# Kernel tuning notes

Hardware: AMD Instinct MI355X
Metric: run time of the kernel (lower is better)

The kernel has to match this reference:

```python
import jax, jax.numpy as jnp
import numpy as np

N_NODES = 100000
N_EDGES = 1600000
N_FEAT = 128
HIDDEN = 64
N_LAYERS = 3


def setup_inputs() -> dict:
    key = jax.random.key(0)
    ks = jax.random.split(key, 8)
    x = jax.random.normal(ks[0], (N_NODES, N_FEAT), dtype=jnp.float32)
    edge_index = jax.random.randint(ks[1], (2, N_EDGES), 0, N_NODES, dtype=jnp.int64)
    s_emb = 1.0 / np.sqrt(N_FEAT)
    s_h = 1.0 / np.sqrt(HIDDEN)
    W_emb = jax.random.uniform(ks[2], (N_FEAT, HIDDEN), jnp.float32, -s_emb, s_emb)
    b_emb = jax.random.uniform(ks[3], (HIDDEN,), jnp.float32, -s_emb, s_emb)
    Ws = jax.random.uniform(ks[4], (N_LAYERS, HIDDEN, HIDDEN), jnp.float32, -s_h, s_h)
    bs = jax.random.uniform(ks[5], (N_LAYERS, HIDDEN), jnp.float32, -s_h, s_h)
    return {"x": x, "edge_index": edge_index, "W_emb": W_emb, "b_emb": b_emb,
            "Ws": Ws, "bs": bs}


def gcn_conv(h, src, dst, W, b, deg_inv_sqrt):
    # GCNConv with self-loops and symmetric normalization (PyG semantics):
    # out_i = sum_{j->i} d_i^{-1/2} d_j^{-1/2} (h_j W) + d_i^{-1} (h_i W) + b
    hw = h @ W                                   # [N, H]
    norm = deg_inv_sqrt[src] * deg_inv_sqrt[dst]  # [E]
    msg = hw[src] * norm[:, None]                 # [E, H] gather
    agg = jax.ops.segment_sum(msg, dst, num_segments=N_NODES)  # scatter-add
    agg = agg + hw * (deg_inv_sqrt * deg_inv_sqrt)[:, None]    # self-loop term
    return agg + b


def reference(x, edge_index, W_emb, b_emb, Ws, bs):
    src, dst = edge_index[0], edge_index[1]
    # degree with self-loops (edge weight 1), shared by every layer
    deg = jnp.zeros((N_NODES,), x.dtype).at[dst].add(1.0) + 1.0
    deg_inv_sqrt = jax.lax.rsqrt(deg)

    h = x @ W_emb + b_emb  # embedding Linear
    for i in range(N_LAYERS):
        h = jax.nn.relu(gcn_conv(h, src, dst, Ws[i], bs[i], deg_inv_sqrt))
    return h
```

## Files before the change

kernel.cpp:

```cpp
#include <hip/hip_runtime.h>
#include <hip/hip_fp16.h>
#include <math.h>

#define NN 100000
#define NE 1600000
#define NF 128
#define NH 64
#define NBUCK 196
#define CHA 8192
#define CAP 10240
#define NBLK 1563

typedef _Float16 f16x8 __attribute__((ext_vector_type(8)));
typedef float f32x4 __attribute__((ext_vector_type(4)));

__global__ __launch_bounds__(256) void part_bucket2(const int* __restrict__ src,
                                                    const int* __restrict__ dst,
                                                    int* __restrict__ bcnt,
                                                    int* __restrict__ tmp, int E) {
    __shared__ int hist[NBUCK];
    __shared__ int base[NBUCK];
    int t = threadIdx.x;
    int e0 = blockIdx.x * CHA;
    int e1 = min(e0 + CHA, E);
    if (t < NBUCK) hist[t] = 0;
    __syncthreads();
    for (int i = e0 + t; i < e1; i += 256) {
        atomicAdd(&hist[dst[i] >> 9], 1);
    }
    __syncthreads();
    if (t < NBUCK) {
        int h = hist[t];
        base[t] = h ? atomicAdd(&bcnt[t], h) : 0;
        hist[t] = 0;
    }
    __syncthreads();
    for (int i = e0 + t; i < e1; i += 256) {
        int d = dst[i];
        int b = d >> 9;
        int r = atomicAdd(&hist[b], 1);
        tmp[b * CAP + base[b] + r] = ((d & 511) << 17) | src[i];
    }
}

__global__ __launch_bounds__(256) void scan_buckets(const int* __restrict__ bcnt,
                                                    int* __restrict__ cbase,
                                                    int* __restrict__ rowptr) {
    __shared__ int s[256];
    int t = threadIdx.x;
    s[t] = (t < NBUCK) ? bcnt[t] : 0;
    __syncthreads();
    for (int off = 1; off < 256; off <<= 1) {
        int v = (t >= off) ? s[t - off] : 0;
        __syncthreads();
        s[t] += v;
        __syncthreads();
    }
    if (t < NBUCK) cbase[t] = (t == 0) ? 0 : s[t - 1];
    if (t == 0) rowptr[NN] = NE;
}

__global__ __launch_bounds__(256) void bucket_finalize(const int* __restrict__ bcnt,
                                                       const int* __restrict__ cbase,
                                                       const int* __restrict__ tmp,
                                                       int* __restrict__ rowptr,
                                                       float* __restrict__ dsq,
                                                       int* __restrict__ csr_src) {
    __shared__ int ebuf[CAP];
    __shared__ int hcnt[512];
    __shared__ int hoff[512];
    __shared__ int s[256];
    int b = blockIdx.x, t = threadIdx.x;
    int cb = bcnt[b];
    int base = cbase[b];
    const int* tsrc = tmp + b * CAP;
    for (int i = t; i < cb; i += 256) ebuf[i] = tsrc[i];
    hcnt[t] = 0;
    hcnt[t + 256] = 0;
    __syncthreads();
    for (int i = t; i < cb; i += 256) atomicAdd(&hcnt[ebuf[i] >> 17], 1);
    __syncthreads();
    int c0 = hcnt[2 * t], c1 = hcnt[2 * t + 1];
    s[t] = c0 + c1;
    __syncthreads();
    for (int off = 1; off < 256; off <<= 1) {
        int v = (t >= off) ? s[t - off] : 0;
        __syncthreads();
        s[t] += v;
        __syncthreads();
    }
    int pb = (t == 0) ? 0 : s[t - 1];
    hoff[2 * t] = pb;
    hoff[2 * t + 1] = pb + c0;
    __syncthreads();
    int nodelo = b << 9;
    int nnodes = min(512, NN - nodelo);
    for (int i = t; i < nnodes; i += 256) {
        rowptr[nodelo + i] = base + hoff[i];
        dsq[nodelo + i] = rsqrtf((float)hcnt[i] + 1.0f);
    }
    __syncthreads();
    for (int i = t; i < cb; i += 256) {
        int e = ebuf[i];
        int dlow = e >> 17;
        int p = atomicAdd(&hoff[dlow], 1);
        csr_src[base + p] = e & 0x1FFFF;
    }
}

__global__ __launch_bounds__(256) void combine_w(const float* __restrict__ We,
                                                 const float* __restrict__ be,
                                                 const float* __restrict__ W0,
                                                 _Float16* __restrict__ Wct,
                                                 float* __restrict__ bc) {
    __shared__ float w0[NH * NH];
    int t = threadIdx.x;
    for (int i = t; i < NH * NH; i += 256) w0[i] = W0[i];
    __syncthreads();
    int row = blockIdx.x * 4 + (t >> 6);
    int col = t & 63;
    float a = 0.f;
#pragma unroll 8
    for (int k = 0; k < NH; ++k) a += We[row * NH + k] * w0[k * NH + col];
    Wct[col * NF + row] = (_Float16)a;
    if (blockIdx.x == 0 && t < NH) {
        float s = 0.f;
        for (int k = 0; k < NH; ++k) s += be[k] * w0[k * NH + t];
        bc[t] = s;
    }
}

__global__ __launch_bounds__(256) void wconv(const float* __restrict__ W,
                                             _Float16* __restrict__ Wt) {
    int i = blockIdx.x * 256 + threadIdx.x;
    int k = i >> 6, c = i & 63;
    Wt[c * NH + k] = (_Float16)W[i];
}

__global__ __launch_bounds__(256) void fuse0_gemm(const float* __restrict__ x,
                                                  const _Float16* __restrict__ Wct,
                                                  const float* __restrict__ bc,
                                                  const float* __restrict__ dsq,
                                                  __half* __restrict__ hws) {
    __shared__ _Float16 sh[64 * NF];
    int t = threadIdx.x;
    int lane = t & 63;
    int w = t >> 6;
    int row0 = blockIdx.x * 64;

    f16x8 bf[4][4];
#pragma unroll
    for (int ct = 0; ct < 4; ++ct)
#pragma unroll
        for (int ks = 0; ks < 4; ++ks) {
            int col = ct * 16 + (lane & 15);
            int k = ks * 32 + (lane >> 4) * 8;
            bf[ct][ks] = *(const f16x8*)(Wct + col * NF + k);
        }

    const float4* xs = (const float4*)x;
#pragma unroll
    for (int i = 0; i < 8; ++i) {
        int f = t + i * 256;
        int r = f >> 5;
        int c4 = f & 31;
        int row = min(row0 + r, NN - 1);
        float4 v = xs[(size_t)row * 32 + c4];
        __half2 h0 = __floats2half2_rn(v.x, v.y);
        __half2 h1 = __floats2half2_rn(v.z, v.w);
        uint2 u;
        u.x = *(unsigned*)&h0;
        u.y = *(unsigned*)&h1;
        int byte = (r * 256 + c4 * 8) ^ ((r & 7) << 4);
        *(uint2*)((char*)sh + byte) = u;
    }
    __syncthreads();

    f32x4 acc[4] = {{0.f, 0.f, 0.f, 0.f}, {0.f, 0.f, 0.f, 0.f},
                    {0.f, 0.f, 0.f, 0.f}, {0.f, 0.f, 0.f, 0.f}};
    int ar = w * 16 + (lane & 15);
    int ak = (lane >> 4) * 8;
#pragma unroll
    for (int ks = 0; ks < 4; ++ks) {
        int byte = (ar * 256 + (ks * 32 + ak) * 2) ^ ((ar & 7) << 4);
        f16x8 af = *(const f16x8*)((const char*)sh + byte);
#pragma unroll
        for (int ct = 0; ct < 4; ++ct)
            acc[ct] = __builtin_amdgcn_mfma_f32_16x16x32_f16(af, bf[ct][ks], acc[ct], 0, 0, 0);
    }
#pragma unroll
    for (int ct = 0; ct < 4; ++ct) {
        int col = ct * 16 + (lane & 15);
        float bcv = bc[col];
#pragma unroll
        for (int r2 = 0; r2 < 4; ++r2) {
            int row = row0 + w * 16 + (lane >> 4) * 4 + r2;
            if (row < NN)
                hws[(size_t)row * NH + col] = __float2half((acc[ct][r2] + bcv) * dsq[row]);
        }
    }
}

__global__ __launch_bounds__(256) void layer_gemm(const __half* __restrict__ h,
                                                  const _Float16* __restrict__ Wt,
                                                  const float* __restrict__ dsq,
                                                  __half* __restrict__ hws) {
    __shared__ _Float16 sh[64 * NH];
    int t = threadIdx.x;
    int lane = t & 63;
    int w = t >> 6;
    int row0 = blockIdx.x * 64;

    f16x8 bf[4][2];
#pragma unroll
    for (int ct = 0; ct < 4; ++ct)
#pragma unroll
        for (int ks = 0; ks < 2; ++ks) {
            int col = ct * 16 + (lane & 15);
            int k = ks * 32 + (lane >> 4) * 8;
            bf[ct][ks] = *(const f16x8*)(Wt + col * NH + k);
        }

#pragma unroll
    for (int i = 0; i < 2; ++i) {
        int u = t + i * 256;
        int r = u >> 3;
        int c8 = u & 7;
        int row = min(row0 + r, NN - 1);
        uint4 v = *(const uint4*)(h + (size_t)row * NH + c8 * 8);
        int byte = (r * 128 + c8 * 16) ^ ((r & 7) << 4);
        *(uint4*)((char*)sh + byte) = v;
    }
    __syncthreads();

    f32x4 acc[4] = {{0.f, 0.f, 0.f, 0.f}, {0.f, 0.f, 0.f, 0.f},
                    {0.f, 0.f, 0.f, 0.f}, {0.f, 0.f, 0.f, 0.f}};
    int ar = w * 16 + (lane & 15);
    int ak = (lane >> 4) * 8;
#pragma unroll
    for (int ks = 0; ks < 2; ++ks) {
        int byte = (ar * 128 + (ks * 32 + ak) * 2) ^ ((ar & 7) << 4);
        f16x8 af = *(const f16x8*)((const char*)sh + byte);
#pragma unroll
        for (int ct = 0; ct < 4; ++ct)
            acc[ct] = __builtin_amdgcn_mfma_f32_16x16x32_f16(af, bf[ct][ks], acc[ct], 0, 0, 0);
    }
#pragma unroll
    for (int ct = 0; ct < 4; ++ct) {
        int col = ct * 16 + (lane & 15);
#pragma unroll
        for (int r2 = 0; r2 < 4; ++r2) {
            int row = row0 + w * 16 + (lane >> 4) * 4 + r2;
            if (row < NN)
                hws[(size_t)row * NH + col] = __float2half(acc[ct][r2] * dsq[row]);
        }
    }
}

#define ADDROWM(sidx, m)                                                     \
    {                                                                        \
        uint4 rv = *(const uint4*)(hws_in + (size_t)(sidx) * NH + fl);       \
        float2 f0 = __half22float2(*(const __half2*)&rv.x);                  \
        float2 f1 = __half22float2(*(const __half2*)&rv.y);                  \
        float2 f2 = __half22float2(*(const __half2*)&rv.z);                  \
        float2 f3 = __half22float2(*(const __half2*)&rv.w);                  \
        a0 += f0.x * (m); a1 += f0.y * (m); a2 += f1.x * (m); a3 += f1.y * (m); \
        a4 += f2.x * (m); a5 += f2.y * (m); a6 += f3.x * (m); a7 += f3.y * (m); \
    }

#define GATHER_BODY                                                          \
    int t = threadIdx.x;                                                     \
    int node = blockIdx.x * 4 + (t >> 6);                                    \
    int lane = t & 63;                                                       \
    int g = lane >> 3;                                                       \
    int fl = (lane & 7) << 3;                                                \
    int beg = rowptr[node], end = rowptr[node + 1];                          \
    int deg = end - beg;                                                     \
    float a0 = 0.f, a1 = 0.f, a2 = 0.f, a3 = 0.f;                            \
    float a4 = 0.f, a5 = 0.f, a6 = 0.f, a7 = 0.f;                            \
    if (g == 0) ADDROWM(node, 1.f);                                          \
    int idxl = csr_src[min(beg + lane, NE - 1)];                             \
    _Pragma("unroll")                                                        \
    for (int k = 0; k < 8; ++k) {                                            \
        if (k * 8 < deg) {                                                   \
            int e = k * 8 + g;                                               \
            int s_ = __shfl(idxl, min(e, deg - 1));                          \
            float m = (e < deg) ? 1.f : 0.f;                                 \
            ADDROWM(s_, m);                                                  \
        }                                                                    \
    }                                                                        \
    for (int jb = beg + 64; jb < end; jb += 64) {       \
        int rem = end - jb;                                                  \
        int idx2 = csr_src[min(jb + lane, NE - 1)];                          \
        _Pragma("unroll")                                                    \
        for (int k = 0; k < 8; ++k) {                                        \
            if (k * 8 < rem) {                                               \
                int e = k * 8 + g;                                           \
                int s_ = __shfl(idx2, min(e, rem - 1));                      \
                float m = (e < rem) ? 1.f : 0.f;                             \
                ADDROWM(s_, m);                                              \
            }                                                                \
        }                                                                    \
    }                                                                        \
    a0 += __shfl_xor(a0, 8);  a1 += __shfl_xor(a1, 8);                       \
    a2 += __shfl_xor(a2, 8);  a3 += __shfl_xor(a3, 8);                       \
    a4 += __shfl_xor(a4, 8);  a5 += __shfl_xor(a5, 8);                       \
    a6 += __shfl_xor(a6, 8);  a7 += __shfl_xor(a7, 8);                       \
    a0 += __shfl_xor(a0, 16); a1 += __shfl_xor(a1, 16);                      \
    a2 += __shfl_xor(a2, 16); a3 += __shfl_xor(a3, 16);                      \
    a4 += __shfl_xor(a4, 16); a5 += __shfl_xor(a5, 16);                      \
    a6 += __shfl_xor(a6, 16); a7 += __shfl_xor(a7, 16);                      \
    a0 += __shfl_xor(a0, 32); a1 += __shfl_xor(a1, 32);                      \
    a2 += __shfl_xor(a2, 32); a3 += __shfl_xor(a3, 32);                      \
    a4 += __shfl_xor(a4, 32); a5 += __shfl_xor(a5, 32);                      \
    a6 += __shfl_xor(a6, 32); a7 += __shfl_xor(a7, 32);

__global__ __launch_bounds__(256) void gather_h(const int* __restrict__ rowptr,
                                                const int* __restrict__ csr_src,
                                                const __half* __restrict__ hws_in,
                                                const float* __restrict__ dsq,
                                                const float* __restrict__ b,
                                                __half* __restrict__ hout) {
    GATHER_BODY
    if (lane < 8) {
        float ds = dsq[node];
        float4 b0 = *(const float4*)(b + fl);
        float4 b1 = *(const float4*)(b + fl + 4);
        __half2 o[4];
        o[0] = __floats2half2_rn(fmaxf(ds * a0 + b0.x, 0.f), fmaxf(ds * a1 + b0.y, 0.f));
        o[1] = __floats2half2_rn(fmaxf(ds * a2 + b0.z, 0.f), fmaxf(ds * a3 + b0.w, 0.f));
        o[2] = __floats2half2_rn(fmaxf(ds * a4 + b1.x, 0.f), fmaxf(ds * a5 + b1.y, 0.f));
        o[3] = __floats2half2_rn(fmaxf(ds * a6 + b1.z, 0.f), fmaxf(ds * a7 + b1.w, 0.f));
        *(uint4*)(hout + (size_t)node * NH + fl) = *(const uint4*)o;
    }
}

__global__ __launch_bounds__(256) void gather_out(const int* __restrict__ rowptr,
                                                  const int* __restrict__ csr_src,
                                                  const __half* __restrict__ hws_in,
                                                  const float* __restrict__ dsq,
                                                  const float* __restrict__ b,
                                                  float* __restrict__ outbuf) {
    GATHER_BODY
    if (lane < 8) {
        float ds = dsq[node];
        float4 b0 = *(const float4*)(b + fl);
        float4 b1 = *(const float4*)(b + fl + 4);
        float4 o0, o1;
        o0.x = fmaxf(ds * a0 + b0.x, 0.f);
        o0.y = fmaxf(ds * a1 + b0.y, 0.f);
        o0.z = fmaxf(ds * a2 + b0.z, 0.f);
        o0.w = fmaxf(ds * a3 + b0.w, 0.f);
        o1.x = fmaxf(ds * a4 + b1.x, 0.f);
        o1.y = fmaxf(ds * a5 + b1.y, 0.f);
        o1.z = fmaxf(ds * a6 + b1.z, 0.f);
        o1.w = fmaxf(ds * a7 + b1.w, 0.f);
        *(float4*)(outbuf + (size_t)node * NH + fl) = o0;
        *(float4*)(outbuf + (size_t)node * NH + fl + 4) = o1;
    }
}

extern "C" void kernel_launch(void* const* d_in, const int* in_sizes, int n_in,
                              void* d_out, int out_size, void* d_ws, size_t ws_size,
                              hipStream_t stream) {
    const float* x     = (const float*)d_in[0];
    const int*   ei    = (const int*)d_in[1];
    const float* W_emb = (const float*)d_in[2];
    const float* b_emb = (const float*)d_in[3];
    const float* Ws    = (const float*)d_in[4];
    const float* bs    = (const float*)d_in[5];
    float* out = (float*)d_out;

    const int* src = ei;
    const int* dst = ei + NE;

    char* w = (char*)d_ws;
    int*      bcnt    = (int*)w;              w += 256 * 4;
    int*      cbase   = (int*)w;              w += 256 * 4;
    int*      rowptr  = (int*)w;              w += (NN + 1) * 4;
    float*    dsq     = (float*)w;            w += NN * 4;
    float*    bc      = (float*)w;            w += NH * 4;
    _Float16* Wct     = (_Float16*)w;         w += NF * NH * 2;
    _Float16* Wt1     = (_Float16*)w;         w += NH * NH * 2;
    _Float16* Wt2     = (_Float16*)w;         w += NH * NH * 2;
    int*      csr_src = (int*)w;              w += NE * 4;
    int*      tmp     = (int*)w;              w += (size_t)NBUCK * CAP * 4;
    __half*   Bh      = (__half*)w;           w += (size_t)NN * NH * 2;
    __half*   H16     = (__half*)w;

    hipMemsetAsync(bcnt, 0, 256 * 4, stream);
    part_bucket2<<<(NE + CHA - 1) / CHA, 256, 0, stream>>>(src, dst, bcnt, tmp, NE);
    scan_buckets<<<1, 256, 0, stream>>>(bcnt, cbase, rowptr);
    bucket_finalize<<<NBUCK, 256, 0, stream>>>(bcnt, cbase, tmp, rowptr, dsq, csr_src);

    combine_w<<<NF / 4, 256, 0, stream>>>(W_emb, b_emb, Ws, Wct, bc);
    wconv<<<16, 256, 0, stream>>>(Ws + 1 * NH * NH, Wt1);
    wconv<<<16, 256, 0, stream>>>(Ws + 2 * NH * NH, Wt2);

    fuse0_gemm<<<NBLK, 256, 0, stream>>>(x, Wct, bc, dsq, Bh);

    gather_h<<<NN / 4, 256, 0, stream>>>(rowptr, csr_src, Bh, dsq, bs, H16);
    layer_gemm<<<NBLK, 256, 0, stream>>>(H16, Wt1, dsq, Bh);
    gather_h<<<NN / 4, 256, 0, stream>>>(rowptr, csr_src, Bh, dsq, bs + NH, H16);
    layer_gemm<<<NBLK, 256, 0, stream>>>(H16, Wt2, dsq, Bh);
    gather_out<<<NN / 4, 256, 0, stream>>>(rowptr, csr_src, Bh, dsq,
                                           bs + 2 * NH, out);
}
```

Baseline: 280.7 us.

## Narrow gather loads to 8 bytes, merge weight prep kernels, cache dst in LDS

The gather kernels now have each lane load 4 halves (8 bytes) instead of 8 halves, so 16 lanes cover a row and each wave processes 4 edges at a time over 16-edge super-steps. This cuts the cross-lane reduction to two shuffle stages and changes memory access granularity. The intended gain is better latency hiding and less wasted padding on low-degree nodes, at the cost of twice as many load instructions per row. In addition, the three small weight-prep kernels are merged into one launch, and the partition kernel caches dst in shared memory so it is not reloaded in the second pass.

```diff
diff --git a/kernel.cpp b/kernel.cpp
--- a/kernel.cpp
+++ b/kernel.cpp
@@ -20,13 +20,16 @@
                                                     int* __restrict__ tmp, int E) {
     __shared__ int hist[NBUCK];
     __shared__ int base[NBUCK];
+    __shared__ int dbuf[CHA];
     int t = threadIdx.x;
     int e0 = blockIdx.x * CHA;
-    int e1 = min(e0 + CHA, E);
+    int n = min(CHA, E - e0);
     if (t < NBUCK) hist[t] = 0;
     __syncthreads();
-    for (int i = e0 + t; i < e1; i += 256) {
-        atomicAdd(&hist[dst[i] >> 9], 1);
+    for (int i = t; i < n; i += 256) {
+        int d = dst[e0 + i];
+        dbuf[i] = d;
+        atomicAdd(&hist[d >> 9], 1);
     }
     __syncthreads();
     if (t < NBUCK) {
@@ -35,11 +38,11 @@
         hist[t] = 0;
     }
     __syncthreads();
-    for (int i = e0 + t; i < e1; i += 256) {
-        int d = dst[i];
+    for (int i = t; i < n; i += 256) {
+        int d = dbuf[i];
         int b = d >> 9;
         int r = atomicAdd(&hist[b], 1);
-        tmp[b * CAP + base[b] + r] = ((d & 511) << 17) | src[i];
+        tmp[b * CAP + base[b] + r] = ((d & 511) << 17) | src[e0 + i];
     }
 }
 
@@ -108,33 +111,38 @@
     }
 }
 
-__global__ __launch_bounds__(256) void combine_w(const float* __restrict__ We,
-                                                 const float* __restrict__ be,
-                                                 const float* __restrict__ W0,
-                                                 _Float16* __restrict__ Wct,
-                                                 float* __restrict__ bc) {
-    __shared__ float w0[NH * NH];
+__global__ __launch_bounds__(256) void prep_w(const float* __restrict__ We,
+                                              const float* __restrict__ be,
+                                              const float* __restrict__ Ws,
+                                              _Float16* __restrict__ Wct,
+                                              float* __restrict__ bc,
+                                              _Float16* __restrict__ Wt1,
+                                              _Float16* __restrict__ Wt2) {
+    int bb = blockIdx.x;
     int t = threadIdx.x;
-    for (int i = t; i < NH * NH; i += 256) w0[i] = W0[i];
-    __syncthreads();
-    int row = blockIdx.x * 4 + (t >> 6);
-    int col = t & 63;
-    float a = 0.f;
+    if (bb < 32) {
+        __shared__ float w0[NH * NH];
+        for (int i = t; i < NH * NH; i += 256) w0[i] = Ws[i];
+        __syncthreads();
+        int row = bb * 4 + (t >> 6);
+        int col = t & 63;
+        float a = 0.f;
 #pragma unroll 8
-    for (int k = 0; k < NH; ++k) a += We[row * NH + k] * w0[k * NH + col];
-    Wct[col * NF + row] = (_Float16)a;
-    if (blockIdx.x == 0 && t < NH) {
-        float s = 0.f;
-        for (int k = 0; k < NH; ++k) s += be[k] * w0[k * NH + t];
-        bc[t] = s;
-    }
-}
-
-__global__ __launch_bounds__(256) void wconv(const float* __restrict__ W,
-                                             _Float16* __restrict__ Wt) {
-    int i = blockIdx.x * 256 + threadIdx.x;
-    int k = i >> 6, c = i & 63;
-    Wt[c * NH + k] = (_Float16)W[i];
+        for (int k = 0; k < NH; ++k) a += We[row * NH + k] * w0[k * NH + col];
+        Wct[col * NF + row] = (_Float16)a;
+        if (bb == 0 && t < NH) {
+            float s = 0.f;
+            for (int k = 0; k < NH; ++k) s += be[k] * w0[k * NH + t];
+            bc[t] = s;
+        }
+    } else {
+        int which = (bb - 32) >> 4;
+        int i = ((bb - 32) & 15) * 256 + t;
+        int k = i >> 6, c = i & 63;
+        const float* W = Ws + (which + 1) * NH * NH;
+        _Float16* Wt = which ? Wt2 : Wt1;
+        Wt[c * NH + k] = (_Float16)W[i];
+    }
 }
 
 __global__ __launch_bounds__(256) void fuse0_gemm(const float* __restrict__ x,
@@ -259,61 +267,57 @@
 
 #define ADDROWM(sidx, m)                                                     \
     {                                                                        \
-        uint4 rv = *(const uint4*)(hws_in + (size_t)(sidx) * NH + fl);       \
+        uint2 rv = *(const uint2*)(hws_in + (size_t)(sidx) * NH + fl);       \
         float2 f0 = __half22float2(*(const __half2*)&rv.x);                  \
         float2 f1 = __half22float2(*(const __half2*)&rv.y);                  \
-        float2 f2 = __half22float2(*(const __half2*)&rv.z);                  \
-        float2 f3 = __half22float2(*(const __half2*)&rv.w);                  \
-        a0 += f0.x * (m); a1 += f0.y * (m); a2 += f1.x * (m); a3 += f1.y * (m); \
-        a4 += f2.x * (m); a5 += f2.y * (m); a6 += f3.x * (m); a7 += f3.y * (m); \
+        a0 += f0.x * (m); a1 += f0.y * (m);                                  \
+        a2 += f1.x * (m); a3 += f1.y * (m);                                  \
     }
 
 #define GATHER_BODY                                                          \
     int t = threadIdx.x;                                                     \
     int node = blockIdx.x * 4 + (t >> 6);                                    \
     int lane = t & 63;                                                       \
-    int g = lane >> 3;                                                       \
-    int fl = (lane & 7) << 3;                                                \
+    int g = lane >> 4;                                   \
+    int fl = (lane & 15) << 2;                    \
     int beg = rowptr[node], end = rowptr[node + 1];                          \
     int deg = end - beg;                                                     \
     float a0 = 0.f, a1 = 0.f, a2 = 0.f, a3 = 0.f;                            \
-    float a4 = 0.f, a5 = 0.f, a6 = 0.f, a7 = 0.f;                            \
     if (g == 0) ADDROWM(node, 1.f);                                          \
     int idxl = csr_src[min(beg + lane, NE - 1)];                             \
-    _Pragma("unroll")                                                        \
-    for (int k = 0; k < 8; ++k) {                                            \
-        if (k * 8 < deg) {                                                   \
-            int e = k * 8 + g;                                               \
-            int s_ = __shfl(idxl, min(e, deg - 1));                          \
-            float m = (e < deg) ? 1.f : 0.f;                                 \
-            ADDROWM(s_, m);                                                  \
-        }                                                                    \
-    }                                                                        \
-    for (int jb = beg + 64; jb < end; jb += 64) {       \
-        int rem = end - jb;                                                  \
-        int idx2 = csr_src[min(jb + lane, NE - 1)];                          \
-        _Pragma("unroll")                                                    \
-        for (int k = 0; k < 8; ++k) {                                        \
-            if (k * 8 < rem) {                                               \
-                int e = k * 8 + g;                                           \
-                int s_ = __shfl(idx2, min(e, rem - 1));                      \
-                float m = (e < rem) ? 1.f : 0.f;                             \
+    {                                                                        \
+        int degc = min(deg, 64);                                             \
+        int nsup = (degc + 15) >> 4;                                         \
+        for (int sup = 0; sup < nsup; ++sup) {                               \
+            int eb = sup * 16 + g;                                           \
+            _Pragma("unroll")                                                \
+            for (int q = 0; q < 4; ++q) {                                    \
+                int e = eb + q * 4;                                          \
+                int s_ = __shfl(idxl, min(e, degc - 1));                     \
+                float m = (e < degc) ? 1.f : 0.f;                            \
                 ADDROWM(s_, m);                                              \
             }                                                                \
         }                                                                    \
     }                                                                        \
-    a0 += __shfl_xor(a0, 8);  a1 += __shfl_xor(a1, 8);                       \
-    a2 += __shfl_xor(a2, 8);  a3 += __shfl_xor(a3, 8);                       \
-    a4 += __shfl_xor(a4, 8);  a5 += __shfl_xor(a5, 8);                       \
-    a6 += __shfl_xor(a6, 8);  a7 += __shfl_xor(a7, 8);                       \
+    for (int jb = beg + 64; jb < end; jb += 64) {       \
+        int remc = min(end - jb, 64);                                        \
+        int idx2 = csr_src[min(jb + lane, NE - 1)];                          \
+        int nsup = (remc + 15) >> 4;                                         \
+        for (int sup = 0; sup < nsup; ++sup) {                               \
+            int eb = sup * 16 + g;                                           \
+            _Pragma("unroll")                                                \
+            for (int q = 0; q < 4; ++q) {                                    \
+                int e = eb + q * 4;                                          \
+                int s_ = __shfl(idx2, min(e, remc - 1));                     \
+                float m = (e < remc) ? 1.f : 0.f;                            \
+                ADDROWM(s_, m);                                              \
+            }                                                                \
+        }                                                                    \
+    }                                                                        \
     a0 += __shfl_xor(a0, 16); a1 += __shfl_xor(a1, 16);                      \
     a2 += __shfl_xor(a2, 16); a3 += __shfl_xor(a3, 16);                      \
-    a4 += __shfl_xor(a4, 16); a5 += __shfl_xor(a5, 16);                      \
-    a6 += __shfl_xor(a6, 16); a7 += __shfl_xor(a7, 16);                      \
     a0 += __shfl_xor(a0, 32); a1 += __shfl_xor(a1, 32);                      \
-    a2 += __shfl_xor(a2, 32); a3 += __shfl_xor(a3, 32);                      \
-    a4 += __shfl_xor(a4, 32); a5 += __shfl_xor(a5, 32);                      \
-    a6 += __shfl_xor(a6, 32); a7 += __shfl_xor(a7, 32);
+    a2 += __shfl_xor(a2, 32); a3 += __shfl_xor(a3, 32);
 
 __global__ __launch_bounds__(256) void gather_h(const int* __restrict__ rowptr,
                                                 const int* __restrict__ csr_src,
@@ -322,16 +326,17 @@
                                                 const float* __restrict__ b,
                                                 __half* __restrict__ hout) {
     GATHER_BODY
-    if (lane < 8) {
+    if (lane < 16) {
         float ds = dsq[node];
         float4 b0 = *(const float4*)(b + fl);
-        float4 b1 = *(const float4*)(b + fl + 4);
-        __half2 o[4];
-        o[0] = __floats2half2_rn(fmaxf(ds * a0 + b0.x, 0.f), fmaxf(ds * a1 + b0.y, 0.f));
-        o[1] = __floats2half2_rn(fmaxf(ds * a2 + b0.z, 0.f), fmaxf(ds * a3 + b0.w, 0.f));
-        o[2] = __floats2half2_rn(fmaxf(ds * a4 + b1.x, 0.f), fmaxf(ds * a5 + b1.y, 0.f));
-        o[3] = __floats2half2_rn(fmaxf(ds * a6 + b1.z, 0.f), fmaxf(ds * a7 + b1.w, 0.f));
-        *(uint4*)(hout + (size_t)node * NH + fl) = *(const uint4*)o;
+        __half2 o0 = __floats2half2_rn(fmaxf(ds * a0 + b0.x, 0.f),
+                                       fmaxf(ds * a1 + b0.y, 0.f));
+        __half2 o1 = __floats2half2_rn(fmaxf(ds * a2 + b0.z, 0.f),
+                                       fmaxf(ds * a3 + b0.w, 0.f));
+        uint2 u;
+        u.x = *(unsigned*)&o0;
+        u.y = *(unsigned*)&o1;
+        *(uint2*)(hout + (size_t)node * NH + fl) = u;
     }
 }
 
@@ -342,21 +347,15 @@
                                                   const float* __restrict__ b,
                                                   float* __restrict__ outbuf) {
     GATHER_BODY
-    if (lane < 8) {
+    if (lane < 16) {
         float ds = dsq[node];
         float4 b0 = *(const float4*)(b + fl);
-        float4 b1 = *(const float4*)(b + fl + 4);
-        float4 o0, o1;
-        o0.x = fmaxf(ds * a0 + b0.x, 0.f);
-        o0.y = fmaxf(ds * a1 + b0.y, 0.f);
-        o0.z = fmaxf(ds * a2 + b0.z, 0.f);
-        o0.w = fmaxf(ds * a3 + b0.w, 0.f);
-        o1.x = fmaxf(ds * a4 + b1.x, 0.f);
-        o1.y = fmaxf(ds * a5 + b1.y, 0.f);
-        o1.z = fmaxf(ds * a6 + b1.z, 0.f);
-        o1.w = fmaxf(ds * a7 + b1.w, 0.f);
-        *(float4*)(outbuf + (size_t)node * NH + fl) = o0;
-        *(float4*)(outbuf + (size_t)node * NH + fl + 4) = o1;
+        float4 o;
+        o.x = fmaxf(ds * a0 + b0.x, 0.f);
+        o.y = fmaxf(ds * a1 + b0.y, 0.f);
+        o.z = fmaxf(ds * a2 + b0.z, 0.f);
+        o.w = fmaxf(ds * a3 + b0.w, 0.f);
+        *(float4*)(outbuf + (size_t)node * NH + fl) = o;
     }
 }
 
@@ -393,9 +392,7 @@
     scan_buckets<<<1, 256, 0, stream>>>(bcnt, cbase, rowptr);
     bucket_finalize<<<NBUCK, 256, 0, stream>>>(bcnt, cbase, tmp, rowptr, dsq, csr_src);
 
-    combine_w<<<NF / 4, 256, 0, stream>>>(W_emb, b_emb, Ws, Wct, bc);
-    wconv<<<16, 256, 0, stream>>>(Ws + 1 * NH * NH, Wt1);
-    wconv<<<16, 256, 0, stream>>>(Ws + 2 * NH * NH, Wt2);
+    prep_w<<<64, 256, 0, stream>>>(W_emb, b_emb, Ws, Wct, bc, Wt1, Wt2);
 
     fuse0_gemm<<<NBLK, 256, 0, stream>>>(x, Wct, bc, dsq, Bh);
 
```

Measured after the change: 266.1 us. 5.2% less time.
